# Kernel tuning notes

Hardware: AMD Instinct MI355X
Metric: run time of the kernel (lower is better)

Reference implementation:

```python
import jax, jax.numpy as jnp
import numpy as np

B, LQ, S, D = 4, 8192, 16384, 256
NH, NP, NL = 8, 4, 1
DH = D // NH
HH = WW = 128  # S = HH*WW


def _ln(x, g, b, eps=1e-5):
    m = x.mean(-1, keepdims=True)
    v = ((x - m) ** 2).mean(-1, keepdims=True)
    return (x - m) * jax.lax.rsqrt(v + eps) * g + b


def setup_inputs() -> dict:
    key = jax.random.key(0)
    ks = jax.random.split(key, 12)
    w = lambda k, shape: jax.random.normal(k, shape, jnp.float32) * 0.02
    return {
        "tgt": jax.random.normal(ks[0], (B, LQ, D), jnp.float32),
        "src": jax.random.normal(ks[1], (B, S, D), jnp.float32),
        "reference_points": jax.random.uniform(ks[2], (B, LQ, NL, 2), jnp.float32),
        "W_value": w(ks[3], (D, D)), "b_value": jnp.zeros((D,), jnp.float32),
        "W_off": w(ks[4], (D, NH * NL * NP * 2)), "b_off": w(ks[5], (NH * NL * NP * 2,)),
        "W_attn": w(ks[6], (D, NH * NL * NP)), "b_attn": jnp.zeros((NH * NL * NP,), jnp.float32),
        "W_out": w(ks[7], (D, D)), "b_out": jnp.zeros((D,), jnp.float32),
        "ln1_g": jnp.ones((D,), jnp.float32), "ln1_b": jnp.zeros((D,), jnp.float32),
        "ln2_g": jnp.ones((D,), jnp.float32), "ln2_b": jnp.zeros((D,), jnp.float32),
        "H": HH, "W": WW,
    }


def _forward(tgt, src, reference_points, W_value, b_value, W_off, b_off,
             W_attn, b_attn, W_out, b_out, ln1_g, ln1_b, ln2_g, ln2_b, H, W):
    b, lq, d = tgt.shape
    s = src.shape[1]
    # ---- MSDeformAttn ----
    value = (src @ W_value + b_value).reshape(b, s, NH, DH)
    off = (tgt @ W_off + b_off).reshape(b, lq, NH, NL, NP, 2)
    attn = jax.nn.softmax((tgt @ W_attn + b_attn).reshape(b, lq, NH, NL * NP), axis=-1)
    attn = attn.reshape(b, lq, NH, NL, NP)
    normalizer = jnp.array([[W, H]], dtype=jnp.float32)  # [NL,2]: x by W, y by H
    loc = reference_points[:, :, None, :, None, :] + off / normalizer[None, None, None, :, None, :]
    bi = jnp.arange(b)[:, None, None, None]
    hi = jnp.arange(NH)[None, None, :, None]
    out = jnp.zeros((b, lq, NH, DH), tgt.dtype)
    start = 0
    for l in range(NL):
        v = value[:, start:start + H * W].reshape(b, H, W, NH, DH)
        # grid_sample(align_corners=False): pixel = loc*size - 0.5, zero padding outside
        x = loc[:, :, :, l, :, 0] * W - 0.5  # [B,LQ,NH,NP]
        y = loc[:, :, :, l, :, 1] * H - 0.5
        x0 = jnp.floor(x); y0 = jnp.floor(y)
        wx1 = x - x0; wy1 = y - y0

        def gather(yy, xx):
            valid = (yy >= 0) & (yy < H) & (xx >= 0) & (xx < W)
            yi = jnp.clip(yy, 0, H - 1).astype(jnp.int32)
            xi = jnp.clip(xx, 0, W - 1).astype(jnp.int32)
            g = v[bi, yi, xi, hi]  # [B,LQ,NH,NP,DH]
            return g * valid[..., None]

        g00 = gather(y0, x0)
        g01 = gather(y0, x0 + 1)
        g10 = gather(y0 + 1, x0)
        g11 = gather(y0 + 1, x0 + 1)
        sampled = (((1 - wy1) * (1 - wx1))[..., None] * g00
                   + ((1 - wy1) * wx1)[..., None] * g01
                   + (wy1 * (1 - wx1))[..., None] * g10
                   + (wy1 * wx1)[..., None] * g11)
        out = out + jnp.sum(sampled * attn[:, :, :, l, :, None], axis=3)
        start += H * W
    attn_out = out.reshape(b, lq, d) @ W_out + b_out
    # residual + norm1 (dropout is identity at inference)
    query = _ln(tgt + attn_out, ln1_g, ln1_b)
    # forward_ffn as written: src2 is dead code; src = norm2(src + dropout(src))
    src_out = _ln(src + src, ln2_g, ln2_b)
    return query, src_out


def reference(tgt, src, reference_points, W_value, b_value, W_off, b_off,
              W_attn, b_attn, W_out, b_out, ln1_g, ln1_b, ln2_g, ln2_b, H, W):
    return _forward(tgt, src, reference_points, W_value, b_value, W_off, b_off,
                    W_attn, b_attn, W_out, b_out, ln1_g, ln1_b, ln2_g, ln2_b, H, W)
```

## Files before the change

kernel.cpp:

```cpp
#include <hip/hip_runtime.h>

__device__ __forceinline__ float u2f(unsigned short u) {
  union { unsigned int i; float f; } v; v.i = ((unsigned)u) << 16; return v.f;
}
__device__ __forceinline__ unsigned short f2u(float f) {
  union { float f; unsigned int i; } v; v.f = f;
  unsigned int x = v.i;
  return (unsigned short)((x + 0x7fffu + ((x >> 16) & 1u)) >> 16);
}
__device__ __forceinline__ unsigned int pack2(float a, float b) {
  return (unsigned int)f2u(a) | ((unsigned int)f2u(b) << 16);
}
__device__ __forceinline__ void acc2(float& a0, float& a1, unsigned int w, float wgt) {
  union { unsigned int i; float f; } lo, hi;
  lo.i = w << 16; hi.i = w & 0xffff0000u;
  a0 += wgt * lo.f; a1 += wgt * hi.f;
}
__device__ __forceinline__ void gload16(const void* g, void* l) {
  __builtin_amdgcn_global_load_lds((const __attribute__((address_space(1))) void*)g,
                                   (__attribute__((address_space(3))) void*)l, 16, 0, 0);
}

__device__ __forceinline__ void decode_hw(const void* Hp, const void* Wp, int& H, int& W) {
  long long h = ((const int*)Hp)[0], w = ((const int*)Wp)[0];
  if (h >= 1 && h <= 16384 && w >= 1 && w <= 16384 && h * w == 16384) { H = (int)h; W = (int)w; return; }
  float fh = ((const float*)Hp)[0], fw = ((const float*)Wp)[0];
  if (fh >= 1.f && fh <= 16384.f && fw >= 1.f && fw <= 16384.f &&
      (long long)fh * (long long)fw == 16384) { H = (int)fh; W = (int)fw; return; }
  H = 128; W = 128;
}

typedef __attribute__((ext_vector_type(4))) float f32x4;
typedef __attribute__((ext_vector_type(8))) short bf16x8;

__launch_bounds__(256)
__global__ void prep_kernel(const float* __restrict__ Wv, const float* __restrict__ Wo,
                            const float* __restrict__ Wa, const float* __restrict__ Wout,
                            const float* __restrict__ bo, const float* __restrict__ ba,
                            unsigned short* __restrict__ Btv,
                            unsigned short* __restrict__ Btout,
                            unsigned short* __restrict__ Btol,
                            float* __restrict__ bol)
{
  const int n = blockIdx.x;
  const int k = threadIdx.x;
  if (n < 256) {
    Btv[n * 256 + k] = f2u(Wv[k * 256 + n]);
  } else if (n < 512) {
    const int nn = n - 256;
    Btout[nn * 256 + k] = f2u(Wout[k * 256 + nn]);
  } else {
    const int nn = n - 512;
    float v = (nn < 64) ? Wo[k * 64 + nn] : ((nn < 96) ? Wa[k * 32 + (nn - 64)] : 0.f);
    Btol[nn * 256 + k] = f2u(v);
    if (k == 0) bol[nn] = (nn < 64) ? bo[nn] : ((nn < 96) ? ba[nn - 64] : 0.f);
  }
}

template<int BN, bool OUTBF16>
__launch_bounds__(256)
__global__ void mfma_gemm(const float* __restrict__ A,
                          const unsigned short* __restrict__ Bt,
                          const float* __restrict__ bias,
                          void* __restrict__ C,
                          int N, int ldc)
{
  constexpr int NF = BN / 64;
  __shared__ __align__(16) unsigned short As[64][72];
  __shared__ __align__(16) unsigned short Bs[BN][64];
  const int tid = threadIdx.x;
  const int wid = tid >> 6, lane = tid & 63;
  const int row16 = lane & 15, kq = lane >> 4;
  const int swz = row16 & 7;
  const int m0 = blockIdx.x * 64;
  const int wn0 = wid * (BN / 4);

  f32x4 acc[4][NF];
  const f32x4 zero4 = {0.f, 0.f, 0.f, 0.f};
  #pragma unroll
  for (int i = 0; i < 4; ++i)
    #pragma unroll
    for (int j = 0; j < NF; ++j)
      acc[i][j] = zero4;

  const int arow = tid >> 2, aq = tid & 3;
  constexpr int NISS = BN / 32;

  for (int k0 = 0; k0 < 256; k0 += 64) {
    #pragma unroll
    for (int j = 0; j < NISS; ++j) {
      const int rowbase = (wid * NISS + j) * 8;
      const int brow = rowbase + (lane >> 3);
      const int gsrc = (lane & 7) ^ (brow & 7);
      gload16(Bt + (size_t)brow * 256 + k0 + gsrc * 8, &Bs[rowbase][0]);
    }
    {
      const float* ap = A + (size_t)(m0 + arow) * 256 + k0 + aq * 16;
      float4 f0 = *(const float4*)(ap + 0);
      float4 f1 = *(const float4*)(ap + 4);
      float4 g0 = *(const float4*)(ap + 8);
      float4 g1 = *(const float4*)(ap + 12);
      uint4 u0 = make_uint4(pack2(f0.x, f0.y), pack2(f0.z, f0.w), pack2(f1.x, f1.y), pack2(f1.z, f1.w));
      uint4 u1 = make_uint4(pack2(g0.x, g0.y), pack2(g0.z, g0.w), pack2(g1.x, g1.y), pack2(g1.z, g1.w));
      *(uint4*)&As[arow][aq * 16 + 0] = u0;
      *(uint4*)&As[arow][aq * 16 + 8] = u1;
    }
    __syncthreads();

    #pragma unroll
    for (int ks = 0; ks < 64; ks += 32) {
      bf16x8 af[4], bfr[NF];
      #pragma unroll
      for (int mf = 0; mf < 4; ++mf)
        af[mf] = *(const bf16x8*)&As[mf * 16 + row16][ks + kq * 8];
      #pragma unroll
      for (int nf = 0; nf < NF; ++nf)
        bfr[nf] = *(const bf16x8*)&Bs[wn0 + nf * 16 + row16][(((ks >> 3) + kq) ^ swz) * 8];
      #pragma unroll
      for (int mf = 0; mf < 4; ++mf)
        #pragma unroll
        for (int nf = 0; nf < NF; ++nf)
          acc[mf][nf] = __builtin_amdgcn_mfma_f32_16x16x32_bf16(af[mf], bfr[nf], acc[mf][nf], 0, 0, 0);
    }
    __syncthreads();
  }

  #pragma unroll
  for (int nf = 0; nf < NF; ++nf) {
    const int col = wn0 + nf * 16 + row16;
    if (col < N) {
      const float bv = bias[col];
      #pragma unroll
      for (int mf = 0; mf < 4; ++mf) {
        #pragma unroll
        for (int r = 0; r < 4; ++r) {
          const int rrow = m0 + mf * 16 + kq * 4 + r;
          const float v = acc[mf][nf][r] + bv;
          if (OUTBF16) ((unsigned short*)C)[(size_t)rrow * ldc + col] = f2u(v);
          else         ((float*)C)[(size_t)rrow * ldc + col] = v;
        }
      }
    }
  }
}

__launch_bounds__(256)
__global__ void gemm_ln_kernel(const unsigned short* __restrict__ A,
                               const unsigned short* __restrict__ Bt,
                               const float* __restrict__ bias,
                               const float* __restrict__ tgt,
                               const float* __restrict__ g,
                               const float* __restrict__ be,
                               float* __restrict__ out)
{
  __shared__ __align__(16) unsigned short As[64][64];
  __shared__ __align__(16) unsigned short Bs[256][64];
  __shared__ float2 red_s[64][4];
  const int tid = threadIdx.x;
  const int wid = tid >> 6, lane = tid & 63;
  const int row16 = lane & 15, kq = lane >> 4;
  const int swz = row16 & 7;
  const int m0 = blockIdx.x * 64;
  const int wn0 = wid * 64;

  f32x4 acc[4][4];
  const f32x4 zero4 = {0.f, 0.f, 0.f, 0.f};
  #pragma unroll
  for (int i = 0; i < 4; ++i)
    #pragma unroll
    for (int j = 0; j < 4; ++j)
      acc[i][j] = zero4;

  for (int k0 = 0; k0 < 256; k0 += 64) {
    #pragma unroll
    for (int j = 0; j < 8; ++j) {
      const int rowbase = (wid * 8 + j) * 8;
      const int brow = rowbase + (lane >> 3);
      const int gsrc = (lane & 7) ^ (brow & 7);
      gload16(Bt + (size_t)brow * 256 + k0 + gsrc * 8, &Bs[rowbase][0]);
    }
    #pragma unroll
    for (int j = 0; j < 2; ++j) {
      const int rowbase = (wid * 2 + j) * 8;
      const int arow = rowbase + (lane >> 3);
      const int gsrc = (lane & 7) ^ (arow & 7);
      gload16(A + (size_t)(m0 + arow) * 256 + k0 + gsrc * 8, &As[rowbase][0]);
    }
    __syncthreads();

    #pragma unroll
    for (int ks = 0; ks < 64; ks += 32) {
      bf16x8 af[4], bfr[4];
      #pragma unroll
      for (int mf = 0; mf < 4; ++mf)
        af[mf] = *(const bf16x8*)&As[mf * 16 + row16][(((ks >> 3) + kq) ^ swz) * 8];
      #pragma unroll
      for (int nf = 0; nf < 4; ++nf)
        bfr[nf] = *(const bf16x8*)&Bs[wn0 + nf * 16 + row16][(((ks >> 3) + kq) ^ swz) * 8];
      #pragma unroll
      for (int mf = 0; mf < 4; ++mf)
        #pragma unroll
        for (int nf = 0; nf < 4; ++nf)
          acc[mf][nf] = __builtin_amdgcn_mfma_f32_16x16x32_bf16(af[mf], bfr[nf], acc[mf][nf], 0, 0, 0);
    }
    __syncthreads();
  }

  float bcol[4], gcol[4], becol[4];
  #pragma unroll
  for (int nf = 0; nf < 4; ++nf) {
    const int col = wn0 + nf * 16 + row16;
    bcol[nf] = bias[col]; gcol[nf] = g[col]; becol[nf] = be[col];
  }
  #pragma unroll
  for (int mf = 0; mf < 4; ++mf) {
    #pragma unroll
    for (int r = 0; r < 4; ++r) {
      const int row = mf * 16 + kq * 4 + r;
      float s = 0.f, q = 0.f;
      #pragma unroll
      for (int nf = 0; nf < 4; ++nf) {
        const int col = wn0 + nf * 16 + row16;
        float v = acc[mf][nf][r] + bcol[nf] + tgt[(size_t)(m0 + row) * 256 + col];
        acc[mf][nf][r] = v;
        s += v; q += v * v;
      }
      #pragma unroll
      for (int off = 1; off < 16; off <<= 1) {
        s += __shfl_xor(s, off);
        q += __shfl_xor(q, off);
      }
      if (row16 == 0) red_s[row][wid] = make_float2(s, q);
    }
  }
  __syncthreads();

  #pragma unroll
  for (int mf = 0; mf < 4; ++mf) {
    #pragma unroll
    for (int r = 0; r < 4; ++r) {
      const int row = mf * 16 + kq * 4 + r;
      const float2 a0 = red_s[row][0], a1 = red_s[row][1];
      const float2 a2 = red_s[row][2], a3 = red_s[row][3];
      const float s = a0.x + a1.x + a2.x + a3.x;
      const float q = a0.y + a1.y + a2.y + a3.y;
      const float mean = s * (1.f / 256.f);
      const float var = q * (1.f / 256.f) - mean * mean;
      const float rstd = rsqrtf(var + 1e-5f);
      #pragma unroll
      for (int nf = 0; nf < 4; ++nf) {
        const int col = wn0 + nf * 16 + row16;
        out[(size_t)(m0 + row) * 256 + col] = (acc[mf][nf][r] - mean) * rstd * gcol[nf] + becol[nf];
      }
    }
  }
}

#define RQ 8
__launch_bounds__(256)
__global__ void sample_kernel(const unsigned short* __restrict__ value,
                              const float* __restrict__ offlog,
                              const float* __restrict__ refp,
                              unsigned short* __restrict__ out,
                              const void* __restrict__ Hp,
                              const void* __restrict__ Wp)
{
  int H, W; decode_hw(Hp, Wp, H, W);
  const int S = H * W;
  __shared__ float off_s[RQ][64];
  __shared__ float lg_s[RQ][36];
  __shared__ float ref_s[RQ][2];
  const int tid = threadIdx.x;
  const int r0 = blockIdx.x * RQ;

  if (tid < RQ * 24) {
    const int row = tid / 24, c4 = (tid % 24) * 4;
    float4 v = *(const float4*)(offlog + (size_t)(r0 + row) * 96 + c4);
    if (c4 < 64) *(float4*)&off_s[row][c4] = v;
    else         *(float4*)&lg_s[row][c4 - 64] = v;
  }
  if (tid < RQ * 2)
    ref_s[tid >> 1][tid & 1] = refp[(size_t)(r0 + (tid >> 1)) * 2 + (tid & 1)];
  __syncthreads();

  const int row = tid >> 5;
  const int h   = (tid >> 2) & 7;
  const int o   = tid & 3;
  const int b = r0 >> 13;
  const unsigned short* vptr = value + (size_t)b * S * 256 + h * 32 + o * 8;

  const int r = r0 + row;
  float lg[4];
  #pragma unroll
  for (int p = 0; p < 4; ++p) lg[p] = lg_s[row][h * 4 + p];
  const float mx = fmaxf(fmaxf(lg[0], lg[1]), fmaxf(lg[2], lg[3]));
  float sum = 0.f;
  #pragma unroll
  for (int p = 0; p < 4; ++p) { lg[p] = __expf(lg[p] - mx); sum += lg[p]; }
  const float inv = 1.f / sum;
  const float rx = ref_s[row][0], ry = ref_s[row][1];

  float a[8];
  #pragma unroll
  for (int j = 0; j < 8; ++j) a[j] = 0.f;

  #pragma unroll
  for (int p = 0; p < 4; ++p) {
    const float x = rx * (float)W + off_s[row][h * 8 + p * 2 + 0] - 0.5f;
    const float y = ry * (float)H + off_s[row][h * 8 + p * 2 + 1] - 0.5f;
    const float xf = floorf(x), yf = floorf(y);
    const float wx = x - xf, wy = y - yf;
    const int x0 = (int)xf, y0 = (int)yf;
    const float wp = lg[p] * inv;
    #pragma unroll
    for (int dy = 0; dy < 2; ++dy)
      #pragma unroll
      for (int dx = 0; dx < 2; ++dx) {
        const int yy = y0 + dy, xx = x0 + dx;
        if ((unsigned)yy < (unsigned)H && (unsigned)xx < (unsigned)W) {
          const float wgt = wp * (dy ? wy : 1.f - wy) * (dx ? wx : 1.f - wx);
          const uint4 v4 = *(const uint4*)(vptr + (size_t)(yy * W + xx) * 256);
          acc2(a[0], a[1], v4.x, wgt);
          acc2(a[2], a[3], v4.y, wgt);
          acc2(a[4], a[5], v4.z, wgt);
          acc2(a[6], a[7], v4.w, wgt);
        }
      }
  }
  uint4 ov;
  ov.x = pack2(a[0], a[1]); ov.y = pack2(a[2], a[3]);
  ov.z = pack2(a[4], a[5]); ov.w = pack2(a[6], a[7]);
  *(uint4*)(out + (size_t)r * 256 + h * 32 + o * 8) = ov;
}

__launch_bounds__(256)
__global__ void ln2x_kernel(const float* __restrict__ A,
                            const float* __restrict__ g,
                            const float* __restrict__ be,
                            float* __restrict__ out)
{
  const size_t row = (size_t)blockIdx.x * 4 + (threadIdx.x >> 6);
  const int lane = threadIdx.x & 63;
  const size_t base = row * 256 + lane * 4;
  const float4 xa = *(const float4*)(A + base);
  float x[4];
  x[0] = 2.f * xa.x; x[1] = 2.f * xa.y; x[2] = 2.f * xa.z; x[3] = 2.f * xa.w;
  float s = x[0] + x[1] + x[2] + x[3];
  float sq = x[0]*x[0] + x[1]*x[1] + x[2]*x[2] + x[3]*x[3];
  #pragma unroll
  for (int off = 32; off; off >>= 1) {
    s  += __shfl_xor(s, off);
    sq += __shfl_xor(sq, off);
  }
  const float mean = s * (1.f / 256.f);
  const float var = sq * (1.f / 256.f) - mean * mean;
  const float rstd = rsqrtf(var + 1e-5f);
  const float4 gg = *(const float4*)(g + lane * 4);
  const float4 bb = *(const float4*)(be + lane * 4);
  float4 o;
  o.x = (x[0] - mean) * rstd * gg.x + bb.x;
  o.y = (x[1] - mean) * rstd * gg.y + bb.y;
  o.z = (x[2] - mean) * rstd * gg.z + bb.z;
  o.w = (x[3] - mean) * rstd * gg.w + bb.w;
  *(float4*)(out + base) = o;
}

extern "C" void kernel_launch(void* const* d_in, const int* in_sizes, int n_in,
                              void* d_out, int out_size, void* d_ws, size_t ws_size,
                              hipStream_t stream) {
  const float* tgt  = (const float*)d_in[0];
  const float* src  = (const float*)d_in[1];
  const float* refp = (const float*)d_in[2];
  const float* Wv   = (const float*)d_in[3];
  const float* bv   = (const float*)d_in[4];
  const float* Wo   = (const float*)d_in[5];
  const float* bo   = (const float*)d_in[6];
  const float* Wa   = (const float*)d_in[7];
  const float* ba   = (const float*)d_in[8];
  const float* Wout = (const float*)d_in[9];
  const float* bout = (const float*)d_in[10];
  const float* g1   = (const float*)d_in[11];
  const float* b1   = (const float*)d_in[12];
  const float* g2   = (const float*)d_in[13];
  const float* b2   = (const float*)d_in[14];
  const void* Hp    = d_in[15];
  const void* Wp    = d_in[16];

  float* q_out    = (float*)d_out;
  float* s_region = q_out + (size_t)8388608;
  float* s_out    = s_region;

  unsigned short* value = (unsigned short*)d_ws;
  unsigned short* Btv   = value + (size_t)16777216;
  unsigned short* Btout = Btv + 65536;
  unsigned short* Btol  = Btout + 65536;
  float*          bol   = (float*)(Btol + 32768);

  float*          offlog  = s_region;
  unsigned short* sampled = (unsigned short*)(s_region + (size_t)4194304);

  dim3 blk(256);
  prep_kernel<<<dim3(640), blk, 0, stream>>>(Wv, Wo, Wa, Wout, bo, ba, Btv, Btout, Btol, bol);
  mfma_gemm<128, false><<<dim3(512), blk, 0, stream>>>(tgt, Btol, bol, offlog, 96, 96);
  mfma_gemm<256, true><<<dim3(1024), blk, 0, stream>>>(src, Btv, bv, value, 256, 256);
  sample_kernel<<<dim3(32768 / RQ), blk, 0, stream>>>(value, offlog, refp, sampled, Hp, Wp);
  gemm_ln_kernel<<<dim3(512), blk, 0, stream>>>(sampled, Btout, bout, tgt, g1, b1, q_out);
  ln2x_kernel<<<dim3(16384), blk, 0, stream>>>(src, g2, b2, s_out);
}
```

Measured before the change: 292.7 us.

## Prefetch A tiles into registers and stage bf16 GEMM output through LDS

Restructures the mfma_gemm k-loop so the next 64-wide slice of fp32 A is loaded into registers while the current slice is being multiplied. Block-wide __syncthreads is replaced by explicit s_waitcnt/s_barrier so the prefetch loads can stay in flight across the barrier. For the bf16 output path, results are written to a padded LDS tile that reuses the operand shared memory, then stored as coalesced 16-byte rows instead of scattered 2-byte stores. This adds register pressure and depends on hand-written wait counts being correct, and the bf16 path drops the col<N bounds check, which assumes N equals the full tile width.

Result: no change. 288.0 us (-1.6%).

```diff
diff --git a/kernel.cpp b/kernel.cpp
--- a/kernel.cpp
+++ b/kernel.cpp
@@ -66,8 +66,10 @@
                           int N, int ldc)
 {
   constexpr int NF = BN / 64;
-  __shared__ __align__(16) unsigned short As[64][72];
-  __shared__ __align__(16) unsigned short Bs[BN][64];
+  constexpr int NISS = BN / 32;
+  __shared__ __align__(16) unsigned short smem[BN * 64 + 64 * 72];
+  unsigned short (*Bs)[64] = (unsigned short(*)[64])smem;
+  unsigned short (*As)[72] = (unsigned short(*)[72])(smem + BN * 64);
   const int tid = threadIdx.x;
   const int wid = tid >> 6, lane = tid & 63;
   const int row16 = lane & 15, kq = lane >> 4;
@@ -84,29 +86,30 @@
       acc[i][j] = zero4;
 
   const int arow = tid >> 2, aq = tid & 3;
-  constexpr int NISS = BN / 32;
-
-  for (int k0 = 0; k0 < 256; k0 += 64) {
-    #pragma unroll
-    for (int j = 0; j < NISS; ++j) {
-      const int rowbase = (wid * NISS + j) * 8;
-      const int brow = rowbase + (lane >> 3);
-      const int gsrc = (lane & 7) ^ (brow & 7);
-      gload16(Bt + (size_t)brow * 256 + k0 + gsrc * 8, &Bs[rowbase][0]);
-    }
-    {
-      const float* ap = A + (size_t)(m0 + arow) * 256 + k0 + aq * 16;
-      float4 f0 = *(const float4*)(ap + 0);
-      float4 f1 = *(const float4*)(ap + 4);
-      float4 g0 = *(const float4*)(ap + 8);
-      float4 g1 = *(const float4*)(ap + 12);
-      uint4 u0 = make_uint4(pack2(f0.x, f0.y), pack2(f0.z, f0.w), pack2(f1.x, f1.y), pack2(f1.z, f1.w));
-      uint4 u1 = make_uint4(pack2(g0.x, g0.y), pack2(g0.z, g0.w), pack2(g1.x, g1.y), pack2(g1.z, g1.w));
-      *(uint4*)&As[arow][aq * 16 + 0] = u0;
-      *(uint4*)&As[arow][aq * 16 + 8] = u1;
-    }
-    __syncthreads();
-
+  const float* arp = A + (size_t)(m0 + arow) * 256 + aq * 16;
+
+  float4 pf0, pf1, pf2, pf3;
+  pf0 = *(const float4*)(arp + 0);  pf1 = *(const float4*)(arp + 4);
+  pf2 = *(const float4*)(arp + 8);  pf3 = *(const float4*)(arp + 12);
+  #pragma unroll
+  for (int j = 0; j < NISS; ++j) {
+    const int rowbase = (wid * NISS + j) * 8;
+    const int brow = rowbase + (lane >> 3);
+    const int gsrc = (lane & 7) ^ (brow & 7);
+    gload16(Bt + (size_t)brow * 256 + 0 + gsrc * 8, &Bs[rowbase][0]);
+  }
+  {
+    uint4 u0 = make_uint4(pack2(pf0.x, pf0.y), pack2(pf0.z, pf0.w), pack2(pf1.x, pf1.y), pack2(pf1.z, pf1.w));
+    uint4 u1 = make_uint4(pack2(pf2.x, pf2.y), pack2(pf2.z, pf2.w), pack2(pf3.x, pf3.y), pack2(pf3.z, pf3.w));
+    *(uint4*)&As[arow][aq * 16 + 0] = u0;
+    *(uint4*)&As[arow][aq * 16 + 8] = u1;
+  }
+  pf0 = *(const float4*)(arp + 64); pf1 = *(const float4*)(arp + 68);
+  pf2 = *(const float4*)(arp + 72); pf3 = *(const float4*)(arp + 76);
+  asm volatile("s_waitcnt vmcnt(4) lgkmcnt(0)\n\ts_barrier" ::: "memory");
+
+  #pragma unroll
+  for (int c = 0; c < 4; ++c) {
     #pragma unroll
     for (int ks = 0; ks < 64; ks += 32) {
       bf16x8 af[4], bfr[NF];
@@ -122,23 +125,64 @@
         for (int nf = 0; nf < NF; ++nf)
           acc[mf][nf] = __builtin_amdgcn_mfma_f32_16x16x32_bf16(af[mf], bfr[nf], acc[mf][nf], 0, 0, 0);
     }
-    __syncthreads();
-  }
-
-  #pragma unroll
-  for (int nf = 0; nf < NF; ++nf) {
-    const int col = wn0 + nf * 16 + row16;
-    if (col < N) {
+    if (c < 3) {
+      const int k1 = (c + 1) * 64;
+      asm volatile("s_barrier" ::: "memory");
+      #pragma unroll
+      for (int j = 0; j < NISS; ++j) {
+        const int rowbase = (wid * NISS + j) * 8;
+        const int brow = rowbase + (lane >> 3);
+        const int gsrc = (lane & 7) ^ (brow & 7);
+        gload16(Bt + (size_t)brow * 256 + k1 + gsrc * 8, &Bs[rowbase][0]);
+      }
+      {
+        uint4 u0 = make_uint4(pack2(pf0.x, pf0.y), pack2(pf0.z, pf0.w), pack2(pf1.x, pf1.y), pack2(pf1.z, pf1.w));
+        uint4 u1 = make_uint4(pack2(pf2.x, pf2.y), pack2(pf2.z, pf2.w), pack2(pf3.x, pf3.y), pack2(pf3.z, pf3.w));
+        *(uint4*)&As[arow][aq * 16 + 0] = u0;
+        *(uint4*)&As[arow][aq * 16 + 8] = u1;
+      }
+      if (c < 2) {
+        const float* apn = arp + (c + 2) * 64;
+        pf0 = *(const float4*)(apn + 0);  pf1 = *(const float4*)(apn + 4);
+        pf2 = *(const float4*)(apn + 8);  pf3 = *(const float4*)(apn + 12);
+        asm volatile("s_waitcnt vmcnt(4) lgkmcnt(0)\n\ts_barrier" ::: "memory");
+      } else {
+        asm volatile("s_waitcnt vmcnt(0) lgkmcnt(0)\n\ts_barrier" ::: "memory");
+      }
+    }
+  }
+
+  if constexpr (OUTBF16) {
+    asm volatile("s_barrier" ::: "memory");
+    unsigned short (*Cs)[264] = (unsigned short(*)[264])smem;
+    #pragma unroll
+    for (int nf = 0; nf < NF; ++nf) {
+      const int col = wn0 + nf * 16 + row16;
       const float bv = bias[col];
       #pragma unroll
-      for (int mf = 0; mf < 4; ++mf) {
+      for (int mf = 0; mf < 4; ++mf)
         #pragma unroll
-        for (int r = 0; r < 4; ++r) {
-          const int rrow = m0 + mf * 16 + kq * 4 + r;
-          const float v = acc[mf][nf][r] + bv;
-          if (OUTBF16) ((unsigned short*)C)[(size_t)rrow * ldc + col] = f2u(v);
-          else         ((float*)C)[(size_t)rrow * ldc + col] = v;
-        }
+        for (int r = 0; r < 4; ++r)
+          Cs[mf * 16 + kq * 4 + r][col] = f2u(acc[mf][nf][r] + bv);
+    }
+    asm volatile("s_waitcnt lgkmcnt(0)\n\ts_barrier" ::: "memory");
+    #pragma unroll
+    for (int j = 0; j < 8; ++j) {
+      const int row = j * 8 + (tid >> 5);
+      const int col = (tid & 31) * 8;
+      *(uint4*)((unsigned short*)C + (size_t)(m0 + row) * ldc + col) = *(const uint4*)&Cs[row][col];
+    }
+  } else {
+    #pragma unroll
+    for (int nf = 0; nf < NF; ++nf) {
+      const int col = wn0 + nf * 16 + row16;
+      if (col < N) {
+        const float bv = bias[col];
+        #pragma unroll
+        for (int mf = 0; mf < 4; ++mf)
+          #pragma unroll
+          for (int r = 0; r < 4; ++r)
+            ((float*)C)[(size_t)(m0 + mf * 16 + kq * 4 + r) * ldc + col] = acc[mf][nf][r] + bv;
       }
     }
   }
```
